# Performance work log

Hardware: AMD Instinct MI355X
Metric: run time of the kernel (lower is better)

## Reference

```python
import jax, jax.numpy as jnp
import numpy as np

BS, L, D, N, K = 2048, 100, 256, 16, 32
M_CONST = 2
NEG = -1e9


def setup_inputs() -> dict:
    key = jax.random.key(0)
    ks = jax.random.split(key, 6)
    hist = jax.random.normal(ks[0], (BS, L, D), dtype=jnp.float32)
    hist_mask = jnp.ones((BS, L), dtype=jnp.float32)  # passed but unused by PolyAttention (faithful)
    cand = jax.random.normal(ks[1], (BS, N, D), dtype=jnp.float32)
    num_interests = jax.random.randint(ks[2], (BS,), 1, K + 1, dtype=jnp.int32)
    cat_counts = jax.random.randint(ks[3], (BS,), 1, 21, dtype=jnp.int32)
    W_poly = jax.random.normal(ks[4], (D, D), dtype=jnp.float32) * (1.0 / np.sqrt(D))
    context_codes = jax.random.normal(ks[5], (K, D), dtype=jnp.float32) * (1.0 / np.sqrt(D))
    return {
        "history_news_representations": hist,
        "history_mask": hist_mask,
        "candidate_news_representations": cand,
        "num_extracted_interests": num_interests,
        "unique_category_counts": cat_counts,
        "W_poly": W_poly,
        "context_codes": context_codes,
    }


def _forward(hist, hist_mask, cand, num_interests, cat_counts, W_poly, context_codes):
    # --- PolyAttention ---
    proj = jnp.tanh(jnp.einsum("bld,ed->ble", hist, W_poly))        # [bs, L, ccd]
    weights = jnp.einsum("ble,ke->bkl", proj, context_codes)         # [bs, K, L]
    cc_mask = jnp.arange(K)[None, :] < num_interests[:, None]        # [bs, K]
    weights = jnp.where(cc_mask[:, :, None], weights, NEG)
    weights = jax.nn.softmax(weights, axis=2)
    weights = jnp.nan_to_num(weights, nan=0.0, posinf=0.0, neginf=0.0)
    interests = jnp.einsum("bkl,bld->bkd", weights, hist)            # [bs, K, d]

    # --- InterestCandidateAttention over all N candidates at once ---
    aw = jnp.einsum("bkd,bnd->bnk", interests, cand)                 # [bs, N, K]
    dyn_K = jnp.ceil(jnp.log2(M_CONST * cat_counts.astype(jnp.float32))).astype(jnp.int32)
    dyn_K = jnp.clip(dyn_K, 1, K)                                    # [bs]
    # rank of each entry in descending order along K
    order = jnp.argsort(-aw, axis=-1)
    rank = jnp.argsort(order, axis=-1)                               # [bs, N, K]
    topk_mask = (rank < dyn_K[:, None, None]).astype(aw.dtype)
    masked = aw * topk_mask
    user = jnp.einsum("bnk,bkd->bnd", masked, interests)             # [bs, N, d]
    return user


def reference(history_news_representations, history_mask, candidate_news_representations,
              num_extracted_interests, unique_category_counts, W_poly, context_codes):
    return _forward(history_news_representations, history_mask, candidate_news_representations,
                    num_extracted_interests, unique_category_counts, W_poly, context_codes)
```

## Files before the change

kernel.cpp:

```cpp
#include <hip/hip_runtime.h>
#include <math.h>

#define NEGV (-1e9f)

typedef _Float16 half8 __attribute__((ext_vector_type(8)));
typedef float f32x4 __attribute__((ext_vector_type(4)));


__device__ inline float tanh_fast(float x) {
    float t = __expf(2.0f * x);
    float r = __builtin_amdgcn_rcpf(t + 1.0f);
    return fmaf(-2.0f, r, 1.0f);
}

__device__ inline void split8(const float4 a, const float4 b, half8& h, half8& m) {
    const float* pa = (const float*)&a;
    const float* pb = (const float*)&b;
    #pragma unroll
    for (int q = 0; q < 4; ++q) {
        float x = pa[q];
        _Float16 hi = (_Float16)x;
        h[q] = hi; m[q] = (_Float16)(x - (float)hi);
    }
    #pragma unroll
    for (int q = 0; q < 4; ++q) {
        float x = pb[q];
        _Float16 hi = (_Float16)x;
        h[4+q] = hi; m[4+q] = (_Float16)(x - (float)hi);
    }
}

__device__ inline void gload_lds16(const void* g, void* lds) {
    __builtin_amdgcn_global_load_lds(
        (const __attribute__((address_space(1))) unsigned int*)g,
        (__attribute__((address_space(3))) unsigned int*)lds, 16, 0, 0);
}

__global__ __launch_bounds__(256)
void k_prep(const float* __restrict__ W, const float* __restrict__ cc,
            half8* __restrict__ Wf, half8* __restrict__ Cf)
{
    int slot = blockIdx.x * 256 + threadIdx.x;
    if (slot < 8192) {
        int kt = slot >> 10;
        int ct = (slot >> 6) & 15;
        int lane = slot & 63;
        int e = ct * 16 + (lane & 15);
        int g = lane >> 4;
        const float* src = &W[(size_t)e * 256 + kt * 32 + g * 8];
        float4 a = *(const float4*)src;
        float4 b = *(const float4*)(src + 4);
        half8 h, m;
        split8(a, b, h, m);
        Wf[((kt * 2 + 0) * 16 + ct) * 64 + lane] = h;
        Wf[((kt * 2 + 1) * 16 + ct) * 64 + lane] = m;
    } else if (slot < 9216) {
        int s = slot - 8192;
        int lane = s & 63;
        int ct = (s >> 6) & 1;
        int et = s >> 7;
        int k2 = ct * 16 + (lane & 15);
        int g = lane >> 4;
        const float* src = &cc[(size_t)k2 * 256 + et * 32 + g * 8];
        float4 a = *(const float4*)src;
        float4 b = *(const float4*)(src + 4);
        half8 h, m;
        split8(a, b, h, m);
        Cf[((et * 2 + 0) * 2 + ct) * 64 + lane] = h;
        Cf[((et * 2 + 1) * 2 + ct) * 64 + lane] = m;
    }
}

__global__ __launch_bounds__(256, 2)
void k_proj_logits(const float* __restrict__ hist, const half8* __restrict__ Wf,
                   const half8* __restrict__ Cf, float* __restrict__ logits)
{
    __shared__ __align__(16) char smem[65536];
    float (*Pj)[68] = (float(*)[68])smem;

    const int tid  = threadIdx.x;
    const int lane = tid & 63;
    const int w    = tid >> 6;
    const int wr   = w >> 1, wc = w & 1;
    const int g    = lane >> 4;
    const int r    = lane & 15;
    const size_t rowBase = (size_t)blockIdx.x * 128;

    f32x4 acc[4][8];
    #pragma unroll
    for (int i = 0; i < 4; ++i)
        #pragma unroll
        for (int j = 0; j < 8; ++j) acc[i][j] = (f32x4)(0.0f);

    const float* aPtr = &hist[(rowBase + (size_t)wr * 64 + r) * 256 + g * 8];
    const char*  wsrc = (const char*)Wf + tid * 16;
    const int    ldsW = (tid & 192) * 16;

    float4 a0[4], a1[4];
    #pragma unroll
    for (int rt = 0; rt < 4; ++rt) {
        const float* s = aPtr + rt * (16 * 256);
        a0[rt] = *(const float4*)s;
        a1[rt] = *(const float4*)(s + 4);
    }
    #pragma unroll
    for (int i = 0; i < 8; ++i)
        gload_lds16(wsrc + i * 4096, smem + ldsW + i * 4096);
    __syncthreads();

    #pragma unroll 2
    for (int kt = 0; kt < 8; ++kt) {
        const int cur = kt & 1;
        if (kt < 7) {
            const char* s = wsrc + (size_t)(kt + 1) * 32768;
            char* d = smem + (cur ^ 1) * 32768 + ldsW;
            #pragma unroll
            for (int i = 0; i < 8; ++i)
                gload_lds16(s + i * 4096, d + i * 4096);
        }
        half8 Ah[4], Am[4];
        #pragma unroll
        for (int rt = 0; rt < 4; ++rt)
            split8(a0[rt], a1[rt], Ah[rt], Am[rt]);
        if (kt < 7) {
            #pragma unroll
            for (int rt = 0; rt < 4; ++rt) {
                const float* s = aPtr + rt * (16 * 256) + (kt + 1) * 32;
                a0[rt] = *(const float4*)s;
                a1[rt] = *(const float4*)(s + 4);
            }
        }
        __builtin_amdgcn_sched_barrier(0);

        const _Float16* Bf = (const _Float16*)(smem + cur * 32768);
        #pragma unroll
        for (int ct = 0; ct < 8; ++ct) {
            int ctg = wc * 8 + ct;
            half8 Bh = *(const half8*)&Bf[(( 0 + ctg) * 64 + lane) * 8];
            half8 Bm = *(const half8*)&Bf[((16 + ctg) * 64 + lane) * 8];
            #pragma unroll
            for (int rt = 0; rt < 4; ++rt) {
                acc[rt][ct] = __builtin_amdgcn_mfma_f32_16x16x32_f16(Ah[rt], Bh, acc[rt][ct], 0, 0, 0);
                acc[rt][ct] = __builtin_amdgcn_mfma_f32_16x16x32_f16(Ah[rt], Bm, acc[rt][ct], 0, 0, 0);
                acc[rt][ct] = __builtin_amdgcn_mfma_f32_16x16x32_f16(Am[rt], Bh, acc[rt][ct], 0, 0, 0);
            }
        }
        __syncthreads();
    }

    f32x4 acc2[2][2];
    #pragma unroll
    for (int i = 0; i < 2; ++i)
        #pragma unroll
        for (int j = 0; j < 2; ++j) acc2[i][j] = (f32x4)(0.0f);

    #pragma unroll
    for (int ec = 0; ec < 4; ++ec) {
        __syncthreads();
        if (wc == (ec >> 1)) {
            #pragma unroll
            for (int rt = 0; rt < 4; ++rt) {
                #pragma unroll
                for (int c4i = 0; c4i < 4; ++c4i) {
                    int ctm = (ec & 1) * 4 + c4i;
                    f32x4 t = acc[rt][ctm];
                    int el = c4i * 16 + r;
                    int rb = 64 * wr + rt * 16 + g * 4;
                    #pragma unroll
                    for (int i = 0; i < 4; ++i)
                        Pj[rb + i][el] = tanh_fast(t[i]);
                }
            }
        }
        __syncthreads();
        #pragma unroll
        for (int ks = 0; ks < 2; ++ks) {
            half8 Ah2[2], Am2[2];
            #pragma unroll
            for (int rt2 = 0; rt2 < 2; ++rt2) {
                const float* src = &Pj[32 * w + rt2 * 16 + r][ks * 32 + g * 8];
                float4 p0 = *(const float4*)src;
                float4 p1 = *(const float4*)(src + 4);
                split8(p0, p1, Ah2[rt2], Am2[rt2]);
            }
            int et = ec * 2 + ks;
            #pragma unroll
            for (int ct = 0; ct < 2; ++ct) {
                half8 Bh = Cf[((et * 2 + 0) * 2 + ct) * 64 + lane];
                half8 Bm = Cf[((et * 2 + 1) * 2 + ct) * 64 + lane];
                #pragma unroll
                for (int rt2 = 0; rt2 < 2; ++rt2) {
                    acc2[rt2][ct] = __builtin_amdgcn_mfma_f32_16x16x32_f16(Ah2[rt2], Bh, acc2[rt2][ct], 0, 0, 0);
                    acc2[rt2][ct] = __builtin_amdgcn_mfma_f32_16x16x32_f16(Ah2[rt2], Bm, acc2[rt2][ct], 0, 0, 0);
                    acc2[rt2][ct] = __builtin_amdgcn_mfma_f32_16x16x32_f16(Am2[rt2], Bh, acc2[rt2][ct], 0, 0, 0);
                }
            }
        }
    }
    #pragma unroll
    for (int rt2 = 0; rt2 < 2; ++rt2)
        #pragma unroll
        for (int ct = 0; ct < 2; ++ct)
            #pragma unroll
            for (int i = 0; i < 4; ++i) {
                size_t grow = rowBase + 32 * w + rt2 * 16 + g * 4 + i;
                logits[grow * 32 + ct * 16 + r] = acc2[rt2][ct][i];
            }
}

__global__ __launch_bounds__(256, 3)
void k_attn(const float* __restrict__ hist, const float* __restrict__ cand,
            const int* __restrict__ numi, const int* __restrict__ catc,
            const float* __restrict__ logits, float* __restrict__ out)
{
    __shared__ float wT[100][36];
    __shared__ float ints[32][260];
    __shared__ float aws[16][36];
    __shared__ float maw[16][36];

    const int tid = threadIdx.x;
    const int b = blockIdx.x;
    const int num = numi[b];

    for (int idx = tid; idx < 3200; idx += 256) {
        int l = idx >> 5;
        int k = idx & 31;
        wT[l][k] = logits[(size_t)b * 3200 + idx];
    }
    __syncthreads();

    {
        const int k = tid >> 3;
        const int lg = tid & 7;
        const bool valid = k < num;
        float vals[13];
        float m = -INFINITY;
        #pragma unroll
        for (int i = 0; i < 13; ++i) {
            int l = lg + 8 * i;
            if (l < 100) {
                float v = valid ? wT[l][k] : NEGV;
                vals[i] = v;
                m = fmaxf(m, v);
            }
        }
        #pragma unroll
        for (int off = 1; off < 8; off <<= 1)
            m = fmaxf(m, __shfl_xor(m, off, 8));
        float s = 0.0f;
        #pragma unroll
        for (int i = 0; i < 13; ++i) {
            int l = lg + 8 * i;
            if (l < 100) {
                float e = expf(vals[i] - m);
                s += e;
                wT[l][k] = e;
            }
        }
        #pragma unroll
        for (int off = 1; off < 8; off <<= 1)
            s += __shfl_xor(s, off, 8);
        float inv = 1.0f / s;
        #pragma unroll
        for (int i = 0; i < 13; ++i) {
            int l = lg + 8 * i;
            if (l < 100) wT[l][k] *= inv;
        }
    }
    __syncthreads();

    {
        const int dq = tid & 63;
        const int kh = tid >> 6;
        float4 a4[8];
        #pragma unroll
        for (int kk = 0; kk < 8; ++kk) { a4[kk].x = a4[kk].y = a4[kk].z = a4[kk].w = 0.0f; }
        const float4* hrow = (const float4*)&hist[(size_t)b * 25600] + dq;
        #pragma unroll 4
        for (int l = 0; l < 100; ++l) {
            float4 hv = hrow[(size_t)l * 64];
            float4 w0 = *(const float4*)&wT[l][8 * kh];
            float4 w1 = *(const float4*)&wT[l][8 * kh + 4];
            float wv[8] = {w0.x, w0.y, w0.z, w0.w, w1.x, w1.y, w1.z, w1.w};
            #pragma unroll
            for (int kk = 0; kk < 8; ++kk) {
                a4[kk].x = fmaf(wv[kk], hv.x, a4[kk].x);
                a4[kk].y = fmaf(wv[kk], hv.y, a4[kk].y);
                a4[kk].z = fmaf(wv[kk], hv.z, a4[kk].z);
                a4[kk].w = fmaf(wv[kk], hv.w, a4[kk].w);
            }
        }
        #pragma unroll
        for (int kk = 0; kk < 8; ++kk)
            *(float4*)&ints[8 * kh + kk][4 * dq] = a4[kk];
    }
    __syncthreads();

    {
        const int n = tid & 15;
        const int kq = tid >> 4;
        const float4* cg = (const float4*)&cand[((size_t)b * 16 + n) * 256];
        const float4* i0 = (const float4*)&ints[kq][0];
        const float4* i1 = (const float4*)&ints[kq + 16][0];
        float s0 = 0.0f, s1 = 0.0f;
        for (int q = 0; q < 64; ++q) {
            float4 cv = cg[q];
            float4 v0 = i0[q];
            float4 v1 = i1[q];
            s0 += v0.x * cv.x + v0.y * cv.y + v0.z * cv.z + v0.w * cv.w;
            s1 += v1.x * cv.x + v1.y * cv.y + v1.z * cv.z + v1.w * cv.w;
        }
        aws[n][kq] = s0;
        aws[n][kq + 16] = s1;
    }
    __syncthreads();

    {
        int c = catc[b];
        int dynK = 32 - __clz(2 * c - 1);
        const int k = tid & 31;
        const int n1 = tid >> 5;
        #pragma unroll
        for (int h = 0; h < 2; ++h) {
            int n = n1 + 8 * h;
            float a = aws[n][k];
            int cnt = 0;
            #pragma unroll
            for (int j = 0; j < 32; ++j) {
                float aj = aws[n][j];
                cnt += (aj > a) || (aj == a && j < k);
            }
            maw[n][k] = (cnt < dynK) ? a : 0.0f;
        }
    }
    __syncthreads();

    {
        const int dd = tid & 63;
        const int ng = tid >> 6;
        float4 acc4[4];
        #pragma unroll
        for (int nn = 0; nn < 4; ++nn) { acc4[nn].x = acc4[nn].y = acc4[nn].z = acc4[nn].w = 0.0f; }
        for (int k = 0; k < 32; ++k) {
            float4 iv = *(const float4*)&ints[k][4 * dd];
            #pragma unroll
            for (int nn = 0; nn < 4; ++nn) {
                float m = maw[4 * ng + nn][k];
                acc4[nn].x = fmaf(m, iv.x, acc4[nn].x);
                acc4[nn].y = fmaf(m, iv.y, acc4[nn].y);
                acc4[nn].z = fmaf(m, iv.z, acc4[nn].z);
                acc4[nn].w = fmaf(m, iv.w, acc4[nn].w);
            }
        }
        #pragma unroll
        for (int nn = 0; nn < 4; ++nn) {
            *(float4*)&out[((size_t)b * 16 + 4 * ng + nn) * 256 + 4 * dd] = acc4[nn];
        }
    }
}

extern "C" void kernel_launch(void* const* d_in, const int* in_sizes, int n_in,
                              void* d_out, int out_size, void* d_ws, size_t ws_size,
                              hipStream_t stream) {
    const float* hist = (const float*)d_in[0];
    const float* cand = (const float*)d_in[2];
    const int*   numi = (const int*)d_in[3];
    const int*   catc = (const int*)d_in[4];
    const float* W    = (const float*)d_in[5];
    const float* cc   = (const float*)d_in[6];
    float* out = (float*)d_out;
    float* logits = (float*)d_ws;
    const size_t LOG_BYTES = 26214400;
    const size_t WF_BYTES = 262144;
    const size_t CF_BYTES = 32768;
    char* fragBase = (ws_size >= LOG_BYTES + WF_BYTES + CF_BYTES)
                     ? ((char*)d_ws + LOG_BYTES)
                     : (char*)d_out;
    half8* Wf = (half8*)fragBase;
    half8* Cf = (half8*)(fragBase + WF_BYTES);

    k_prep<<<36, 256, 0, stream>>>(W, cc, Wf, Cf);
    k_proj_logits<<<1600, 256, 0, stream>>>(hist, Wf, Cf, logits);
    k_attn<<<2048, 256, 0, stream>>>(hist, cand, numi, catc, logits, out);
}
```

Measured before the change: 233.0 us.

## Fuse projection/logits and attention kernels into one per-batch kernel

Merges the projection+logits kernel with the attention kernel so each block handles one batch row of 100 history items. Logits stay in shared memory instead of going through a global workspace round trip, and the second read of hist for the interest computation may hit cache. It also masks out the padded row tiles beyond 100, which wastes some MFMA tile capacity. The cost is a larger LDS footprint (about 80KB per block), which may reduce occupancy, and 2048 heavier blocks in place of 1600 plus 2048 lighter ones.

```diff
diff --git a/kernel.cpp b/kernel.cpp
--- a/kernel.cpp
+++ b/kernel.cpp
@@ -72,11 +72,17 @@
 }
 
 __global__ __launch_bounds__(256, 2)
-void k_proj_logits(const float* __restrict__ hist, const half8* __restrict__ Wf,
-                   const half8* __restrict__ Cf, float* __restrict__ logits)
+void k_fused(const float* __restrict__ hist, const float* __restrict__ cand,
+             const int* __restrict__ numi, const int* __restrict__ catc,
+             const half8* __restrict__ Wf, const half8* __restrict__ Cf,
+             float* __restrict__ out)
 {
-    __shared__ __align__(16) char smem[65536];
-    float (*Pj)[68] = (float(*)[68])smem;
+    __shared__ __align__(16) char smemA[65536 + 14400];
+    float (*Pj)[68]   = (float(*)[68])smemA;
+    float (*ints)[260] = (float(*)[260])smemA;
+    float (*aws)[36]  = (float(*)[36])(smemA + 33280);
+    float (*maw)[36]  = (float(*)[36])(smemA + 35584);
+    float (*wT)[36]   = (float(*)[36])(smemA + 65536);
 
     const int tid  = threadIdx.x;
     const int lane = tid & 63;
@@ -84,7 +90,9 @@
     const int wr   = w >> 1, wc = w & 1;
     const int g    = lane >> 4;
     const int r    = lane & 15;
-    const size_t rowBase = (size_t)blockIdx.x * 128;
+    const int b    = blockIdx.x;
+    const size_t rowBase = (size_t)b * 100;
+    const int num = numi[b];
 
     f32x4 acc[4][8];
     #pragma unroll
@@ -95,17 +103,21 @@
     const float* aPtr = &hist[(rowBase + (size_t)wr * 64 + r) * 256 + g * 8];
     const char*  wsrc = (const char*)Wf + tid * 16;
     const int    ldsW = (tid & 192) * 16;
+    const float4 f4z = {0.f, 0.f, 0.f, 0.f};
 
     float4 a0[4], a1[4];
     #pragma unroll
     for (int rt = 0; rt < 4; ++rt) {
-        const float* s = aPtr + rt * (16 * 256);
-        a0[rt] = *(const float4*)s;
-        a1[rt] = *(const float4*)(s + 4);
+        if (rt < 3 || wr == 0) {
+            bool vld = (wr == 0) || (rt < 2) || (r < 4);
+            const float* s = aPtr + rt * (16 * 256);
+            a0[rt] = vld ? *(const float4*)s : f4z;
+            a1[rt] = vld ? *(const float4*)(s + 4) : f4z;
+        } else { a0[rt] = f4z; a1[rt] = f4z; }
     }
     #pragma unroll
     for (int i = 0; i < 8; ++i)
-        gload_lds16(wsrc + i * 4096, smem + ldsW + i * 4096);
+        gload_lds16(wsrc + i * 4096, smemA + ldsW + i * 4096);
     __syncthreads();
 
     #pragma unroll 2
@@ -113,7 +125,7 @@
         const int cur = kt & 1;
         if (kt < 7) {
             const char* s = wsrc + (size_t)(kt + 1) * 32768;
-            char* d = smem + (cur ^ 1) * 32768 + ldsW;
+            char* d = smemA + (cur ^ 1) * 32768 + ldsW;
             #pragma unroll
             for (int i = 0; i < 8; ++i)
                 gload_lds16(s + i * 4096, d + i * 4096);
@@ -121,18 +133,22 @@
         half8 Ah[4], Am[4];
         #pragma unroll
         for (int rt = 0; rt < 4; ++rt)
-            split8(a0[rt], a1[rt], Ah[rt], Am[rt]);
+            if (rt < 3 || wr == 0)
+                split8(a0[rt], a1[rt], Ah[rt], Am[rt]);
         if (kt < 7) {
             #pragma unroll
             for (int rt = 0; rt < 4; ++rt) {
-                const float* s = aPtr + rt * (16 * 256) + (kt + 1) * 32;
-                a0[rt] = *(const float4*)s;
-                a1[rt] = *(const float4*)(s + 4);
+                if (rt < 3 || wr == 0) {
+                    bool vld = (wr == 0) || (rt < 2) || (r < 4);
+                    const float* s = aPtr + rt * (16 * 256) + (kt + 1) * 32;
+                    a0[rt] = vld ? *(const float4*)s : f4z;
+                    a1[rt] = vld ? *(const float4*)(s + 4) : f4z;
+                }
             }
         }
         __builtin_amdgcn_sched_barrier(0);
 
-        const _Float16* Bf = (const _Float16*)(smem + cur * 32768);
+        const _Float16* Bf = (const _Float16*)(smemA + cur * 32768);
         #pragma unroll
         for (int ct = 0; ct < 8; ++ct) {
             int ctg = wc * 8 + ct;
@@ -140,9 +156,11 @@
             half8 Bm = *(const half8*)&Bf[((16 + ctg) * 64 + lane) * 8];
             #pragma unroll
             for (int rt = 0; rt < 4; ++rt) {
-                acc[rt][ct] = __builtin_amdgcn_mfma_f32_16x16x32_f16(Ah[rt], Bh, acc[rt][ct], 0, 0, 0);
-                acc[rt][ct] = __builtin_amdgcn_mfma_f32_16x16x32_f16(Ah[rt], Bm, acc[rt][ct], 0, 0, 0);
-                acc[rt][ct] = __builtin_amdgcn_mfma_f32_16x16x32_f16(Am[rt], Bh, acc[rt][ct], 0, 0, 0);
+                if (rt < 3 || wr == 0) {
+                    acc[rt][ct] = __builtin_amdgcn_mfma_f32_16x16x32_f16(Ah[rt], Bh, acc[rt][ct], 0, 0, 0);
+                    acc[rt][ct] = __builtin_amdgcn_mfma_f32_16x16x32_f16(Ah[rt], Bm, acc[rt][ct], 0, 0, 0);
+                    acc[rt][ct] = __builtin_amdgcn_mfma_f32_16x16x32_f16(Am[rt], Bh, acc[rt][ct], 0, 0, 0);
+                }
             }
         }
         __syncthreads();
@@ -160,15 +178,17 @@
         if (wc == (ec >> 1)) {
             #pragma unroll
             for (int rt = 0; rt < 4; ++rt) {
-                #pragma unroll
-                for (int c4i = 0; c4i < 4; ++c4i) {
-                    int ctm = (ec & 1) * 4 + c4i;
-                    f32x4 t = acc[rt][ctm];
-                    int el = c4i * 16 + r;
-                    int rb = 64 * wr + rt * 16 + g * 4;
+                if (rt < 3 || wr == 0) {
                     #pragma unroll
-                    for (int i = 0; i < 4; ++i)
-                        Pj[rb + i][el] = tanh_fast(t[i]);
+                    for (int c4i = 0; c4i < 4; ++c4i) {
+                        int ctm = (ec & 1) * 4 + c4i;
+                        f32x4 t = acc[rt][ctm];
+                        int el = c4i * 16 + r;
+                        int rb = 64 * wr + rt * 16 + g * 4;
+                        #pragma unroll
+                        for (int i = 0; i < 4; ++i)
+                            Pj[rb + i][el] = tanh_fast(t[i]);
+                    }
                 }
             }
         }
@@ -203,30 +223,9 @@
         for (int ct = 0; ct < 2; ++ct)
             #pragma unroll
             for (int i = 0; i < 4; ++i) {
-                size_t grow = rowBase + 32 * w + rt2 * 16 + g * 4 + i;
-                logits[grow * 32 + ct * 16 + r] = acc2[rt2][ct][i];
-            }
-}
-
-__global__ __launch_bounds__(256, 3)
-void k_attn(const float* __restrict__ hist, const float* __restrict__ cand,
-            const int* __restrict__ numi, const int* __restrict__ catc,
-            const float* __restrict__ logits, float* __restrict__ out)
-{
-    __shared__ float wT[100][36];
-    __shared__ float ints[32][260];
-    __shared__ float aws[16][36];
-    __shared__ float maw[16][36];
-
-    const int tid = threadIdx.x;
-    const int b = blockIdx.x;
-    const int num = numi[b];
-
-    for (int idx = tid; idx < 3200; idx += 256) {
-        int l = idx >> 5;
-        int k = idx & 31;
-        wT[l][k] = logits[(size_t)b * 3200 + idx];
-    }
+                int grow = 32 * w + rt2 * 16 + g * 4 + i;
+                if (grow < 100) wT[grow][ct * 16 + r] = acc2[rt2][ct][i];
+            }
     __syncthreads();
 
     {
@@ -275,7 +274,7 @@
         float4 a4[8];
         #pragma unroll
         for (int kk = 0; kk < 8; ++kk) { a4[kk].x = a4[kk].y = a4[kk].z = a4[kk].w = 0.0f; }
-        const float4* hrow = (const float4*)&hist[(size_t)b * 25600] + dq;
+        const float4* hrow = (const float4*)&hist[rowBase * 256] + dq;
         #pragma unroll 4
         for (int l = 0; l < 100; ++l) {
             float4 hv = hrow[(size_t)l * 64];
@@ -369,17 +368,10 @@
     const float* W    = (const float*)d_in[5];
     const float* cc   = (const float*)d_in[6];
     float* out = (float*)d_out;
-    float* logits = (float*)d_ws;
-    const size_t LOG_BYTES = 26214400;
     const size_t WF_BYTES = 262144;
-    const size_t CF_BYTES = 32768;
-    char* fragBase = (ws_size >= LOG_BYTES + WF_BYTES + CF_BYTES)
-                     ? ((char*)d_ws + LOG_BYTES)
-                     : (char*)d_out;
-    half8* Wf = (half8*)fragBase;
-    half8* Cf = (half8*)(fragBase + WF_BYTES);
+    half8* Wf = (half8*)d_ws;
+    half8* Cf = (half8*)((char*)d_ws + WF_BYTES);
 
     k_prep<<<36, 256, 0, stream>>>(W, cc, Wf, Cf);
-    k_proj_logits<<<1600, 256, 0, stream>>>(hist, Wf, Cf, logits);
-    k_attn<<<2048, 256, 0, stream>>>(hist, cand, numi, catc, logits, out);
-}
+    k_fused<<<2048, 256, 0, stream>>>(hist, cand, numi, catc, Wf, Cf, out);
+}
```

After: 245.7 us. +5.4%, slower.

## Double proj-logits block to 512 threads and 256 rows to share W tiles

Applied to the files above, without the earlier changes.

Each k_proj_logits block now covers 256 history rows with 8 waves instead of 128 rows with 4. The LDS-staged W fragments are loaded cooperatively by twice as many threads, so each W tile is reused across twice the rows and global W traffic per row is halved. The tanh/context-code second stage is split into two passes over the shared Pj buffer, each handling 128 rows, with one 16-row tile per wave. The launch bound of 512 threads with 4 blocks per CU may cap registers for the large 4x8 accumulator array and cause spills, and the extra pass adds barriers.

```diff
diff --git a/kernel.cpp b/kernel.cpp
--- a/kernel.cpp
+++ b/kernel.cpp
@@ -71,7 +71,7 @@
     }
 }
 
-__global__ __launch_bounds__(256, 2)
+__global__ __launch_bounds__(512, 4)
 void k_proj_logits(const float* __restrict__ hist, const half8* __restrict__ Wf,
                    const half8* __restrict__ Cf, float* __restrict__ logits)
 {
@@ -84,7 +84,7 @@
     const int wr   = w >> 1, wc = w & 1;
     const int g    = lane >> 4;
     const int r    = lane & 15;
-    const size_t rowBase = (size_t)blockIdx.x * 128;
+    const size_t rowBase = (size_t)blockIdx.x * 256;
 
     f32x4 acc[4][8];
     #pragma unroll
@@ -94,7 +94,7 @@
 
     const float* aPtr = &hist[(rowBase + (size_t)wr * 64 + r) * 256 + g * 8];
     const char*  wsrc = (const char*)Wf + tid * 16;
-    const int    ldsW = (tid & 192) * 16;
+    const int    ldsW = (tid & 448) * 16;
 
     float4 a0[4], a1[4];
     #pragma unroll
@@ -104,8 +104,8 @@
         a1[rt] = *(const float4*)(s + 4);
     }
     #pragma unroll
-    for (int i = 0; i < 8; ++i)
-        gload_lds16(wsrc + i * 4096, smem + ldsW + i * 4096);
+    for (int i = 0; i < 4; ++i)
+        gload_lds16(wsrc + i * 8192, smem + ldsW + i * 8192);
     __syncthreads();
 
     #pragma unroll 2
@@ -115,8 +115,8 @@
             const char* s = wsrc + (size_t)(kt + 1) * 32768;
             char* d = smem + (cur ^ 1) * 32768 + ldsW;
             #pragma unroll
-            for (int i = 0; i < 8; ++i)
-                gload_lds16(s + i * 4096, d + i * 4096);
+            for (int i = 0; i < 4; ++i)
+                gload_lds16(s + i * 8192, d + i * 8192);
         }
         half8 Ah[4], Am[4];
         #pragma unroll
@@ -148,64 +148,58 @@
         __syncthreads();
     }
 
-    f32x4 acc2[2][2];
-    #pragma unroll
-    for (int i = 0; i < 2; ++i)
-        #pragma unroll
-        for (int j = 0; j < 2; ++j) acc2[i][j] = (f32x4)(0.0f);
-
-    #pragma unroll
-    for (int ec = 0; ec < 4; ++ec) {
-        __syncthreads();
-        if (wc == (ec >> 1)) {
-            #pragma unroll
-            for (int rt = 0; rt < 4; ++rt) {
+    #pragma unroll
+    for (int p = 0; p < 2; ++p) {
+        f32x4 acc2[2];
+        acc2[0] = (f32x4)(0.0f);
+        acc2[1] = (f32x4)(0.0f);
+        #pragma unroll
+        for (int ec = 0; ec < 4; ++ec) {
+            __syncthreads();
+            if ((wr >> 1) == p && wc == (ec >> 1)) {
                 #pragma unroll
-                for (int c4i = 0; c4i < 4; ++c4i) {
-                    int ctm = (ec & 1) * 4 + c4i;
-                    f32x4 t = acc[rt][ctm];
-                    int el = c4i * 16 + r;
-                    int rb = 64 * wr + rt * 16 + g * 4;
+                for (int rt = 0; rt < 4; ++rt) {
                     #pragma unroll
-                    for (int i = 0; i < 4; ++i)
-                        Pj[rb + i][el] = tanh_fast(t[i]);
+                    for (int c4i = 0; c4i < 4; ++c4i) {
+                        int ctm = (ec & 1) * 4 + c4i;
+                        f32x4 t = acc[rt][ctm];
+                        int el = c4i * 16 + r;
+                        int rb = (wr & 1) * 64 + rt * 16 + g * 4;
+                        #pragma unroll
+                        for (int i = 0; i < 4; ++i)
+                            Pj[rb + i][el] = tanh_fast(t[i]);
+                    }
                 }
             }
-        }
-        __syncthreads();
-        #pragma unroll
-        for (int ks = 0; ks < 2; ++ks) {
-            half8 Ah2[2], Am2[2];
-            #pragma unroll
-            for (int rt2 = 0; rt2 < 2; ++rt2) {
-                const float* src = &Pj[32 * w + rt2 * 16 + r][ks * 32 + g * 8];
-                float4 p0 = *(const float4*)src;
-                float4 p1 = *(const float4*)(src + 4);
-                split8(p0, p1, Ah2[rt2], Am2[rt2]);
-            }
-            int et = ec * 2 + ks;
-            #pragma unroll
-            for (int ct = 0; ct < 2; ++ct) {
-                half8 Bh = Cf[((et * 2 + 0) * 2 + ct) * 64 + lane];
-                half8 Bm = Cf[((et * 2 + 1) * 2 + ct) * 64 + lane];
+            __syncthreads();
+            #pragma unroll
+            for (int ks = 0; ks < 2; ++ks) {
+                half8 Ah2, Am2;
+                {
+                    const float* src = &Pj[w * 16 + r][ks * 32 + g * 8];
+                    float4 p0 = *(const float4*)src;
+                    float4 p1 = *(const float4*)(src + 4);
+                    split8(p0, p1, Ah2, Am2);
+                }
+                int et = ec * 2 + ks;
                 #pragma unroll
-                for (int rt2 = 0; rt2 < 2; ++rt2) {
-                    acc2[rt2][ct] = __builtin_amdgcn_mfma_f32_16x16x32_f16(Ah2[rt2], Bh, acc2[rt2][ct], 0, 0, 0);
-                    acc2[rt2][ct] = __builtin_amdgcn_mfma_f32_16x16x32_f16(Ah2[rt2], Bm, acc2[rt2][ct], 0, 0, 0);
-                    acc2[rt2][ct] = __builtin_amdgcn_mfma_f32_16x16x32_f16(Am2[rt2], Bh, acc2[rt2][ct], 0, 0, 0);
+                for (int ct = 0; ct < 2; ++ct) {
+                    half8 Bh = Cf[((et * 2 + 0) * 2 + ct) * 64 + lane];
+                    half8 Bm = Cf[((et * 2 + 1) * 2 + ct) * 64 + lane];
+                    acc2[ct] = __builtin_amdgcn_mfma_f32_16x16x32_f16(Ah2, Bh, acc2[ct], 0, 0, 0);
+                    acc2[ct] = __builtin_amdgcn_mfma_f32_16x16x32_f16(Ah2, Bm, acc2[ct], 0, 0, 0);
+                    acc2[ct] = __builtin_amdgcn_mfma_f32_16x16x32_f16(Am2, Bh, acc2[ct], 0, 0, 0);
                 }
             }
         }
-    }
-    #pragma unroll
-    for (int rt2 = 0; rt2 < 2; ++rt2)
         #pragma unroll
         for (int ct = 0; ct < 2; ++ct)
             #pragma unroll
             for (int i = 0; i < 4; ++i) {
-                size_t grow = rowBase + 32 * w + rt2 * 16 + g * 4 + i;
-                logits[grow * 32 + ct * 16 + r] = acc2[rt2][ct][i];
-            }
+                size_t grow = rowBase + p * 128 + w * 16 + g * 4 + i;
+                logits[grow * 32 + ct * 16 + r] = acc2[ct][i];
+            }
+    }
 }
 
 __global__ __launch_bounds__(256, 3)
@@ -380,6 +374,6 @@
     half8* Cf = (half8*)(fragBase + WF_BYTES);
 
     k_prep<<<36, 256, 0, stream>>>(W, cc, Wf, Cf);
-    k_proj_logits<<<1600, 256, 0, stream>>>(hist, Wf, Cf, logits);
+    k_proj_logits<<<800, 512, 0, stream>>>(hist, Wf, Cf, logits);
     k_attn<<<2048, 256, 0, stream>>>(hist, cand, numi, catc, logits, out);
 }
```

Result: slower. 835.9 us (+258.8%).
